# Kernel tuning notes

Hardware: AMD Instinct MI355X
Metric: run time of the kernel (lower is better)

## Reference

```python
import jax, jax.numpy as jnp
import numpy as np

EPS = 1e-8  # torch cosine_similarity eps

def setup_inputs() -> dict:
    key = jax.random.key(0)
    k1, k2 = jax.random.split(key)
    x = jax.random.normal(k1, (256,), dtype=jnp.float32)
    memory = jax.random.uniform(k2, (100000, 256), dtype=jnp.float32)  # torch.rand init
    return {"x": x, "memory": memory}

def reference(x, memory):
    # cosine similarity of query against every memory row (fused batched dot/norm)
    x_norm = jnp.maximum(jnp.linalg.norm(x), EPS)
    mem_norms = jnp.maximum(jnp.linalg.norm(memory, axis=1), EPS)  # [capacity]
    distances = (memory @ x) / (mem_norms * x_norm)               # [capacity]
    argmax = jnp.argmax(distances)
    mask = jax.nn.one_hot(argmax, distances.shape[0], dtype=distances.dtype)
    out = distances * mask
    return out
```

## Files before the change

### kernel.cpp

```cpp
#include <hip/hip_runtime.h>
#include <math.h>


#define EPSF 1e-8f

constexpr int D4     = 64;
constexpr int BLOCK  = 256;
constexpr int NBLK   = 2048;

__device__ __forceinline__ unsigned fkey(float f) {
    unsigned b = __float_as_uint(f);
    return (b & 0x80000000u) ? ~b : (b | 0x80000000u);
}
__device__ __forceinline__ float funkey(unsigned u) {
    unsigned b = (u & 0x80000000u) ? (u & 0x7FFFFFFFu) : ~u;
    return __uint_as_float(b);
}

__global__ __launch_bounds__(BLOCK) void cos_argmax_main(
    const float* __restrict__ x, const float* __restrict__ mem,
    float* __restrict__ out, unsigned long long* __restrict__ part, int nrows)
{
    __shared__ unsigned long long sbest[BLOCK / 64];
    const int lane = threadIdx.x & 63;
    const int wave = threadIdx.x >> 6;

    for (int i = blockIdx.x * BLOCK + threadIdx.x; i < nrows; i += gridDim.x * BLOCK)
        out[i] = 0.0f;

    const float4 xv = reinterpret_cast<const float4*>(x)[lane];
    float xn = xv.x * xv.x + xv.y * xv.y + xv.z * xv.z + xv.w * xv.w;
    #pragma unroll
    for (int off = 32; off; off >>= 1) xn += __shfl_xor(xn, off);
    const float xnorm = fmaxf(sqrtf(xn), EPSF);

    unsigned long long best = 0ull;
    const int gw0     = blockIdx.x * (BLOCK / 64) + wave;
    const int wstride = gridDim.x * (BLOCK / 64);

    for (int row = gw0; row < nrows; row += wstride) {
        const float4 mv = reinterpret_cast<const float4*>(mem)[(size_t)row * D4 + lane];
        float dot = mv.x * xv.x + mv.y * xv.y + mv.z * xv.z + mv.w * xv.w;
        float nrm = mv.x * mv.x + mv.y * mv.y + mv.z * mv.z + mv.w * mv.w;
        #pragma unroll
        for (int off = 32; off; off >>= 1) {
            dot += __shfl_xor(dot, off);
            nrm += __shfl_xor(nrm, off);
        }
        const float dist = dot / (fmaxf(sqrtf(nrm), EPSF) * xnorm);
        const unsigned long long p =
            ((unsigned long long)fkey(dist) << 32) | (unsigned long long)(0xFFFFFFFFu - (unsigned)row);
        best = (p > best) ? p : best;
    }

    if (lane == 0) sbest[wave] = best;
    __syncthreads();
    if (threadIdx.x == 0) {
        unsigned long long b = sbest[0];
        #pragma unroll
        for (int w = 1; w < BLOCK / 64; ++w) b = (sbest[w] > b) ? sbest[w] : b;
        part[blockIdx.x] = b;
    }
}

__global__ __launch_bounds__(BLOCK) void cos_argmax_final(
    const unsigned long long* __restrict__ part, float* __restrict__ out, int nparts)
{
    __shared__ unsigned long long sred[BLOCK];
    unsigned long long best = 0ull;
    for (int i = threadIdx.x; i < nparts; i += BLOCK) {
        const unsigned long long p = part[i];
        best = (p > best) ? p : best;
    }
    sred[threadIdx.x] = best;
    __syncthreads();
    for (int s = BLOCK / 2; s > 0; s >>= 1) {
        if (threadIdx.x < s) {
            const unsigned long long o = sred[threadIdx.x + s];
            if (o > sred[threadIdx.x]) sred[threadIdx.x] = o;
        }
        __syncthreads();
    }
    if (threadIdx.x == 0) {
        const unsigned long long b = sred[0];
        const unsigned idx = 0xFFFFFFFFu - (unsigned)(b & 0xFFFFFFFFull);
        out[idx] = funkey((unsigned)(b >> 32));
    }
}

extern "C" void kernel_launch(void* const* d_in, const int* in_sizes, int n_in,
                              void* d_out, int out_size, void* d_ws, size_t ws_size,
                              hipStream_t stream) {
    const float* x   = (const float*)d_in[0];
    const float* mem = (const float*)d_in[1];
    float* out       = (float*)d_out;
    const int nrows  = in_sizes[1] / 256;
    unsigned long long* part = (unsigned long long*)d_ws;

    cos_argmax_main<<<NBLK, BLOCK, 0, stream>>>(x, mem, out, part, nrows);
    cos_argmax_final<<<1, BLOCK, 0, stream>>>(part, out, NBLK);
}
```

Before: 152.4 us.

## Map 8 lanes per row so each wave processes 8 rows per iteration

Restructures the main kernel so each row is handled by 8 lanes, each loading 8 float4s, and a wave covers 8 rows per step instead of one row per wave. This cuts the shuffle reduction depth per row from 6 to 3 steps and gives each lane more independent loads in flight. The grid is now sized so each wave covers one 8-row group, which for 100k rows gives about 3125 blocks instead of 2048 with grid-stride loops. A wave-level 64-bit max shuffle merges the per-lane best values before the block reduction, and the final kernel reduces over more partials.

New measurement: 154.7 us. About the same (+1.5%).

```diff
diff --git a/kernel.cpp b/kernel.cpp
--- a/kernel.cpp
+++ b/kernel.cpp
@@ -4,9 +4,10 @@
 
 #define EPSF 1e-8f
 
-constexpr int D4     = 64;
-constexpr int BLOCK  = 256;
-constexpr int NBLK   = 2048;
+constexpr int BLOCK = 256;
+constexpr int LPR   = 8;
+constexpr int RPI   = 8;
+constexpr int F4PL  = 8;
 
 __device__ __forceinline__ unsigned fkey(float f) {
     unsigned b = __float_as_uint(f);
@@ -24,35 +25,55 @@
     __shared__ unsigned long long sbest[BLOCK / 64];
     const int lane = threadIdx.x & 63;
     const int wave = threadIdx.x >> 6;
+    const int sub  = lane & (LPR - 1);
+    const int rsub = lane >> 3;
 
     for (int i = blockIdx.x * BLOCK + threadIdx.x; i < nrows; i += gridDim.x * BLOCK)
         out[i] = 0.0f;
 
-    const float4 xv = reinterpret_cast<const float4*>(x)[lane];
-    float xn = xv.x * xv.x + xv.y * xv.y + xv.z * xv.z + xv.w * xv.w;
+    float4 xv[F4PL];
+    float xn = 0.0f;
     #pragma unroll
-    for (int off = 32; off; off >>= 1) xn += __shfl_xor(xn, off);
+    for (int k = 0; k < F4PL; ++k) {
+        xv[k] = reinterpret_cast<const float4*>(x)[sub + LPR * k];
+        xn += xv[k].x * xv[k].x + xv[k].y * xv[k].y + xv[k].z * xv[k].z + xv[k].w * xv[k].w;
+    }
+    #pragma unroll
+    for (int off = 1; off < LPR; off <<= 1) xn += __shfl_xor(xn, off);
     const float xnorm = fmaxf(sqrtf(xn), EPSF);
 
     unsigned long long best = 0ull;
-    const int gw0     = blockIdx.x * (BLOCK / 64) + wave;
-    const int wstride = gridDim.x * (BLOCK / 64);
-
-    for (int row = gw0; row < nrows; row += wstride) {
-        const float4 mv = reinterpret_cast<const float4*>(mem)[(size_t)row * D4 + lane];
-        float dot = mv.x * xv.x + mv.y * xv.y + mv.z * xv.z + mv.w * xv.w;
-        float nrm = mv.x * mv.x + mv.y * mv.y + mv.z * mv.z + mv.w * mv.w;
+    const int nwaves = gridDim.x * (BLOCK / 64);
+    for (int g = blockIdx.x * (BLOCK / 64) + wave; g * RPI < nrows; g += nwaves) {
+        const int row = g * RPI + rsub;
+        float dot = 0.0f, nrm = 0.0f;
+        if (row < nrows) {
+            const float4* rp = reinterpret_cast<const float4*>(mem) + (size_t)row * 64 + sub;
+            #pragma unroll
+            for (int k = 0; k < F4PL; ++k) {
+                const float4 mv = rp[LPR * k];
+                dot += mv.x * xv[k].x + mv.y * xv[k].y + mv.z * xv[k].z + mv.w * xv[k].w;
+                nrm += mv.x * mv.x + mv.y * mv.y + mv.z * mv.z + mv.w * mv.w;
+            }
+        }
         #pragma unroll
-        for (int off = 32; off; off >>= 1) {
+        for (int off = 1; off < LPR; off <<= 1) {
             dot += __shfl_xor(dot, off);
             nrm += __shfl_xor(nrm, off);
         }
-        const float dist = dot / (fmaxf(sqrtf(nrm), EPSF) * xnorm);
-        const unsigned long long p =
-            ((unsigned long long)fkey(dist) << 32) | (unsigned long long)(0xFFFFFFFFu - (unsigned)row);
-        best = (p > best) ? p : best;
+        if (row < nrows) {
+            const float dist = dot / (fmaxf(sqrtf(nrm), EPSF) * xnorm);
+            const unsigned long long p = ((unsigned long long)fkey(dist) << 32)
+                                       | (unsigned long long)(0xFFFFFFFFu - (unsigned)row);
+            best = (p > best) ? p : best;
+        }
     }
 
+    #pragma unroll
+    for (int off = 1; off < 64; off <<= 1) {
+        const unsigned long long o = __shfl_xor(best, off);
+        best = (o > best) ? o : best;
+    }
     if (lane == 0) sbest[wave] = best;
     __syncthreads();
     if (threadIdx.x == 0) {
@@ -97,6 +118,8 @@
     const int nrows  = in_sizes[1] / 256;
     unsigned long long* part = (unsigned long long*)d_ws;
 
-    cos_argmax_main<<<NBLK, BLOCK, 0, stream>>>(x, mem, out, part, nrows);
-    cos_argmax_final<<<1, BLOCK, 0, stream>>>(part, out, NBLK);
+    const int nblk = (nrows + RPI * (BLOCK / 64) - 1) / (RPI * (BLOCK / 64));
+
+    cos_argmax_main<<<nblk, BLOCK, 0, stream>>>(x, mem, out, part, nrows);
+    cos_argmax_final<<<1, BLOCK, 0, stream>>>(part, out, nblk);
 }
```
